# Kernel optimization log

Measured on AMD Instinct MI355X. Metric: run time of the kernel, lower is better.

## Reference

```python
import jax, jax.numpy as jnp
import numpy as np

S = 64        # num_states
ODIM = 8      # padded neighbor-feature width
H = 256       # HIDDEN_DIM
A = 16        # num_actions
B = 16384     # batch (dtpt)
IDIM = S + ODIM
NEG_SLOPE = 0.01  # nn.LeakyReLU default
EPS = 1e-5        # nn.LayerNorm default


def setup_inputs() -> dict:
    key = jax.random.key(0)
    ks = jax.random.split(key, 8)
    x = jax.random.normal(ks[0], (B, S), jnp.float32)
    # per-state neighbor indices into x's feature dim, padded to ODIM with a mask
    o_idx = jax.random.randint(ks[1], (S, ODIM), 0, S)
    o_len = jax.random.randint(ks[2], (S,), 1, ODIM + 1)
    o_mask = jnp.arange(ODIM)[None, :] < o_len[:, None]  # [S, ODIM] bool

    def lin(k, fin, fout):
        bound = 1.0 / np.sqrt(fin)
        kw, kb = jax.random.split(k)
        W = jax.random.uniform(kw, (S, fin, fout), jnp.float32, -bound, bound)
        b = jax.random.uniform(kb, (S, fout), jnp.float32, -bound, bound)
        return W, b

    W1, b1 = lin(ks[3], IDIM, H)
    W2, b2 = lin(ks[4], H, H)
    Wp, bp = lin(ks[5], H, A)
    g1 = jnp.ones((S, H), jnp.float32); be1 = jnp.zeros((S, H), jnp.float32)
    g2 = jnp.ones((S, H), jnp.float32); be2 = jnp.zeros((S, H), jnp.float32)
    return dict(x=x, o_idx=o_idx, o_mask=o_mask, W1=W1, b1=b1, g1=g1, be1=be1,
                W2=W2, b2=b2, g2=g2, be2=be2, Wp=Wp, bp=bp)


def _layer_norm(h, g, b):
    # h: [B, S, H], per-state affine params g,b: [S, H]
    mu = jnp.mean(h, axis=-1, keepdims=True)
    var = jnp.mean((h - mu) ** 2, axis=-1, keepdims=True)
    return (h - mu) * jax.lax.rsqrt(var + EPS) * g[None] + b[None]


def reference(x, o_idx, o_mask, W1, b1, g1, be1, W2, b2, g2, be2, Wp, bp):
    # irregular gather: for each state s take x[:, o_nbr_index[s]], zero-pad to ODIM
    o = jnp.where(o_mask[None, :, :], x[:, o_idx], jnp.float32(0))  # [B, S, ODIM]
    one_hot = jnp.broadcast_to(jnp.eye(S, dtype=x.dtype)[None], (x.shape[0], S, S))
    inp = jnp.concatenate([one_hot, o], axis=-1)  # [B, S, IDIM]

    h = jnp.einsum('bsi,sih->bsh', inp, W1) + b1[None]
    h = _layer_norm(jax.nn.leaky_relu(h, NEG_SLOPE), g1, be1)
    h = jnp.einsum('bsh,shk->bsk', h, W2) + b2[None]
    h = _layer_norm(jax.nn.leaky_relu(h, NEG_SLOPE), g2, be2)
    pi_logit = jnp.einsum('bsh,sha->bsa', h, Wp) + bp[None]  # [B, S, A]
    lg_sm = jax.nn.log_softmax(pi_logit, axis=-1)
    return pi_logit, lg_sm
```

## Files before the change

### kernel.cpp

```cpp
#include <hip/hip_runtime.h>

#define LNEPS 1e-5f

typedef __attribute__((ext_vector_type(8)))  short          bf16x8;
typedef __attribute__((ext_vector_type(8)))  unsigned short u16x8;
typedef __attribute__((ext_vector_type(4)))  float          f32x4;
typedef __attribute__((ext_vector_type(16))) float          f32x16;
typedef __attribute__((ext_vector_type(4)))  unsigned int   u32x4;

#define MFMA32(a, b, c) __builtin_amdgcn_mfma_f32_32x32x16_bf16((a), (b), (c), 0, 0, 0)

#define WS_W2G  0
#define WS_A1   8388608
#define WS_WPG  8912896
#define WS_UC2  10027008
#define WS_MIDX 10092544
#define WS_XG   10094592

union U8 { bf16x8 v; unsigned u[4]; };

__device__ __forceinline__ unsigned short f2bf(float v) {
  union { float f; unsigned u; } a; a.f = v;
  unsigned r = a.u + 0x7fffu + ((a.u >> 16) & 1u);
  return (unsigned short)(r >> 16);
}
__device__ __forceinline__ unsigned cvtpk(float lo, float hi) {
  unsigned r;
  asm("v_cvt_pk_bf16_f32 %0, %1, %2" : "=v"(r) : "v"(lo), "v"(hi));
  return r;
}
__device__ __forceinline__ void swap2(unsigned& a, unsigned& b) {
  asm volatile("v_permlane32_swap_b32 %0, %1" : "+v"(a), "+v"(b));
}

__global__ void prep_midx_k(const int* __restrict__ oidx,
                            const unsigned* __restrict__ mask32,
                            int* __restrict__ midx) {
  __shared__ int fgt1, ffl;
  const int t = threadIdx.x;
  if (t == 0) { fgt1 = 0; ffl = 0; }
  __syncthreads();
  if (t < 128) {
    unsigned wv = mask32[t];
    if (wv == 0x3f800000u) atomicOr(&ffl, 1);
    else if (wv > 1u)      atomicOr(&fgt1, 1);
  }
  __syncthreads();
  const int mode = ffl ? 2 : (fgt1 ? 1 : 0);
  int mv;
  if (mode == 2)      mv = (((const float*)mask32)[t] != 0.0f) ? 1 : 0;
  else if (mode == 1) mv = (int)((const unsigned char*)mask32)[t];
  else                mv = ((const int*)mask32)[t];
  midx[t] = (mv != 0) ? oidx[t] : -1;
}

__global__ __launch_bounds__(256) void prep_xg_k(
    const float* __restrict__ x, const int* __restrict__ midx,
    u32x4* __restrict__ xg) {
  const int g = blockIdx.x * 256 + threadIdx.x;
  const int s = g >> 14, row = g & 16383;
  const float* xr = x + (size_t)row * 64;
  const int* mi = midx + s * 8;
  u32x4 w;
#pragma unroll
  for (int p = 0; p < 4; ++p) {
    const int m0 = mi[2 * p], m1 = mi[2 * p + 1];
    const float a = m0 < 0 ? 0.f : xr[m0];
    const float b = m1 < 0 ? 0.f : xr[m1];
    w[p] = (unsigned)f2bf(a) | ((unsigned)f2bf(b) << 16);
  }
  xg[g] = w;
}

__global__ __launch_bounds__(256) void prep_w2g_k(
    const float* __restrict__ W2, const float* __restrict__ g1,
    unsigned short* __restrict__ w2g) {
  const int tid = blockIdx.x * 256 + threadIdx.x;
  const int l = tid & 63;
  const int t = (tid >> 6) & 15;
  const int i = (tid >> 10) & 7;
  const int s = tid >> 13;
  const int n = i * 32 + (l & 31);
  const int h = l >> 5;
  const float* w = W2 + (size_t)s * 65536;
  const float* g = g1 + s * 256;
  u16x8 v;
#pragma unroll
  for (int j = 0; j < 8; ++j) {
    const int k = t * 16 + h * 8 + j;
    v[j] = f2bf(w[k * 256 + n] * g[k]);
  }
  ((u16x8*)w2g)[tid] = v;
}

__global__ __launch_bounds__(256) void prep_uc2_k(
    const float* __restrict__ W2, const float* __restrict__ g1,
    const float* __restrict__ be1, const float* __restrict__ b2,
    unsigned* __restrict__ uc2) {
  const int tid = blockIdx.x * 256 + threadIdx.x;
  const int s = tid >> 8, n = tid & 255;
  const float* w = W2 + (size_t)s * 65536 + n;
  const float* g = g1 + s * 256;
  const float* be = be1 + s * 256;
  float u = 0.f, c = 0.f;
#pragma unroll 8
  for (int k = 0; k < 256; ++k) {
    const float wk = w[k * 256];
    u = fmaf(wk, g[k], u);
    c = fmaf(wk, be[k], c);
  }
  c += b2[tid];
  uc2[tid] = (unsigned)f2bf(u) | ((unsigned)f2bf(c) << 16);
}

__global__ __launch_bounds__(256) void prep_a1_k(
    const float* __restrict__ W1, const float* __restrict__ b1,
    unsigned short* __restrict__ a1b) {
  const int tid = blockIdx.x * 256 + threadIdx.x;
  const int l = tid & 63;
  const int i = (tid >> 6) & 7;
  const int s = tid >> 9;
  const int n = i * 32 + (l & 31);
  const float* w = W1 + (size_t)s * 72 * 256;
  u16x8 v;
#pragma unroll
  for (int j = 0; j < 8; ++j) v[j] = 0;
  if (l < 32) {
#pragma unroll
    for (int j = 0; j < 8; ++j) v[j] = f2bf(w[(64 + j) * 256 + n]);
  } else {
    v[0] = f2bf(w[s * 256 + n] + b1[s * 256 + n]);
  }
  ((u16x8*)a1b)[tid] = v;
}

__global__ __launch_bounds__(256) void prep_wpg_k(
    const float* __restrict__ Wp, const float* __restrict__ g2,
    const float* __restrict__ be2, const float* __restrict__ bp,
    unsigned short* __restrict__ wpg) {
  const int tid = blockIdx.x * 256 + threadIdx.x;
  const int l = tid & 63;
  const int r = tid >> 6;
  const int t = r % 17;
  const int s = r / 17;
  const int a = l & 31;
  const int h = l >> 5;
  u16x8 v;
#pragma unroll
  for (int j = 0; j < 8; ++j) v[j] = 0;
  if (t < 16) {
    if (a < 16) {
      const float* w = Wp + (size_t)s * 4096;
      const float* g = g2 + s * 256;
#pragma unroll
      for (int j = 0; j < 8; ++j) {
        const int k = t * 16 + h * 8 + j;
        v[j] = f2bf(w[k * 16 + a] * g[k]);
      }
    }
  } else if (h == 0 && a < 16) {
    const float* w = Wp + (size_t)s * 4096;
    float up = 0.f, cp = 0.f;
#pragma unroll 8
    for (int k = 0; k < 256; ++k) {
      const float wk = w[k * 16 + a];
      up = fmaf(wk, g2[s * 256 + k], up);
      cp = fmaf(wk, be2[s * 256 + k], cp);
    }
    cp += bp[s * 16 + a];
    v[0] = f2bf(up); v[1] = f2bf(cp);
  }
  ((u16x8*)wpg)[tid] = v;
}

__device__ __forceinline__ void pack_tile(const f32x16& a,
                                          unsigned* f0, unsigned* f1) {
  unsigned w0 = cvtpk(a[0], a[1]),   w1 = cvtpk(a[2], a[3]);
  unsigned w2 = cvtpk(a[4], a[5]),   w3 = cvtpk(a[6], a[7]);
  unsigned w4 = cvtpk(a[8], a[9]),   w5 = cvtpk(a[10], a[11]);
  unsigned w6 = cvtpk(a[12], a[13]), w7 = cvtpk(a[14], a[15]);
  swap2(w0, w2); swap2(w1, w3); swap2(w4, w6); swap2(w5, w7);
  f0[0] = w0; f0[1] = w1; f0[2] = w2; f0[3] = w3;
  f1[0] = w4; f1[1] = w5; f1[2] = w6; f1[3] = w7;
}

__global__ __launch_bounds__(512, 2) void actor_main(
    const u32x4* __restrict__ xg,
    const unsigned short* __restrict__ w2g, const unsigned* __restrict__ uc2,
    const unsigned short* __restrict__ a1b, const unsigned short* __restrict__ wpg,
    float* __restrict__ out) {
  extern __shared__ char lds[];
  const int tid = threadIdx.x;
  const int wv = tid >> 6;
  const int l = tid & 63;
  const int bl = l & 31;
  const int h = l >> 5;
  const int s = blockIdx.x >> 2;
  const int rowstart = (blockIdx.x & 3) << 12;

  {
    const u32x4* src = (const u32x4*)(w2g + (size_t)s * 65536);
    u32x4* dst = (u32x4*)lds;
#pragma unroll
    for (int i = 0; i < 16; ++i) dst[i * 512 + tid] = src[i * 512 + tid];
  }

  unsigned aext[8];
#pragma unroll
  for (int i = 0; i < 8; ++i) {
    const unsigned t = uc2[(s * 8 + i) * 32 + bl];
    aext[i] = h ? 0u : t;
  }
  const bf16x8* A1 = ((const bf16x8*)a1b) + (size_t)(s * 8) * 64 + l;
  const bf16x8* A3 = ((const bf16x8*)wpg) + (size_t)(s * 17) * 64 + l;
  const char* ldsl = lds + (l << 4);
  const u32x4* XG = xg + ((size_t)s << 14);

  const int rbase = rowstart + wv * 32 + bl;

  u32x4 gcur = XG[rbase];

  __syncthreads();

  for (int it = 0; it < 16; ++it) {
    const int row = rbase + it * 256;

    U8 B1;
    B1.u[0] = h ? 0x00003F80u : gcur[0];
    B1.u[1] = h ? 0u : gcur[1];
    B1.u[2] = h ? 0u : gcur[2];
    B1.u[3] = h ? 0u : gcur[3];

    gcur = XG[rbase + ((it + 1) & 15) * 256];

    float s0 = 0.f, s1 = 0.f, q0 = 0.f, q1 = 0.f;
    f32x16 acc2[8];
    bf16x8 a1n = A1[64];
    bf16x8 Afc[8];
#pragma unroll
    for (int j = 0; j < 8; ++j)
      Afc[j] = *(const bf16x8*)(ldsl + ((j * 16 + 0) << 10));

    f32x16 accP;
    { f32x16 z = {}; accP = MFMA32(A1[0], B1.v, z); }

#pragma unroll
    for (int i = 0; i < 8; ++i) {
      f32x16 yv;
#pragma unroll
      for (int r = 0; r < 16; ++r) {
        float v = accP[r];
        v = fmaxf(v, 0.01f * v);
        yv[r] = v;
        if (r & 1) { s1 += v; q1 = fmaf(v, v, q1); }
        else       { s0 += v; q0 = fmaf(v, v, q0); }
      }
      U8 Bf0, Bf1;
      pack_tile(yv, Bf0.u, Bf1.u);

      if (i < 7) {
        f32x16 z = {};
        accP = MFMA32(a1n, B1.v, z);
        if (i < 6) a1n = A1[(i + 2) * 64];
      }

#pragma unroll
      for (int j = 0; j < 8; ++j) {
        if (i == 0) { f32x16 zz = {}; acc2[j] = MFMA32(Afc[j], Bf0.v, zz); }
        else        { acc2[j] = MFMA32(Afc[j], Bf0.v, acc2[j]); }
      }
      bf16x8 Afn[8];
#pragma unroll
      for (int j = 0; j < 8; ++j)
        Afn[j] = *(const bf16x8*)(ldsl + ((j * 16 + 2 * i + 1) << 10));
#pragma unroll
      for (int j = 0; j < 8; ++j) acc2[j] = MFMA32(Afn[j], Bf1.v, acc2[j]);
      if (i < 7) {
#pragma unroll
        for (int j = 0; j < 8; ++j)
          Afc[j] = *(const bf16x8*)(ldsl + ((j * 16 + 2 * i + 2) << 10));
      }
    }

    float sum = s0 + s1, ssq = q0 + q1;
    sum += __shfl_xor(sum, 32, 64);
    ssq += __shfl_xor(ssq, 32, 64);
    const float m1 = sum * 0.00390625f;
    const float var1 = fmaf(ssq, 0.00390625f, -m1 * m1) + LNEPS;
    const float rho1 = rsqrtf(var1);
    const float std1 = var1 * rho1;
    const unsigned be2w = cvtpk(-m1, std1);
    bf16x8 p0 = A3[0], p1 = A3[64];
    {
      U8 Bx; Bx.u[0] = h ? 0u : be2w; Bx.u[1] = 0; Bx.u[2] = 0; Bx.u[3] = 0;
#pragma unroll
      for (int i = 0; i < 8; ++i) {
        U8 Ax; Ax.u[0] = aext[i]; Ax.u[1] = 0; Ax.u[2] = 0; Ax.u[3] = 0;
        acc2[i] = MFMA32(Ax.v, Bx.v, acc2[i]);
      }
    }

    f32x16 a3a = {}, a3b = {};
    s0 = s1 = q0 = q1 = 0.f;
#pragma unroll
    for (int i = 0; i < 8; ++i) {
      bf16x8 n0, n1;
      if (i < 7) { n0 = A3[(2 * i + 2) * 64]; n1 = A3[(2 * i + 3) * 64]; }
      else       { n0 = A3[16 * 64]; n1 = p1; }
      f32x16 yv;
#pragma unroll
      for (int r = 0; r < 16; ++r) {
        float v = acc2[i][r];
        v = fmaxf(v, 0.01f * v);
        yv[r] = v;
        if (r & 1) { s1 += v; q1 = fmaf(v, v, q1); }
        else       { s0 += v; q0 = fmaf(v, v, q0); }
      }
      U8 Bf0, Bf1;
      pack_tile(yv, Bf0.u, Bf1.u);
      a3a = MFMA32(p0, Bf0.v, a3a);
      a3b = MFMA32(p1, Bf1.v, a3b);
      p0 = n0; p1 = n1;
    }
    float sum2 = s0 + s1, ssq2 = q0 + q1;
    sum2 += __shfl_xor(sum2, 32, 64);
    ssq2 += __shfl_xor(ssq2, 32, 64);
    const float mp = sum2 * 0.00390625f;
    const float qp = ssq2 * 0.00390625f;
    const float var2 = rho1 * rho1 * fmaf(-mp, mp, qp) + LNEPS;
    const float rho2 = rsqrtf(var2);
    const float sigma = rho1 * rho2;
    const float inv = var2 * rho2 * std1;
    const unsigned be3w = cvtpk(-mp, inv);
    {
      U8 Bx; Bx.u[0] = h ? 0u : be3w; Bx.u[1] = 0; Bx.u[2] = 0; Bx.u[3] = 0;
      a3a = MFMA32(p0, Bx.v, a3a);
    }

    float lg[8];
#pragma unroll
    for (int r = 0; r < 8; ++r) lg[r] = sigma * (a3a[r] + a3b[r]);
    float mx = fmaxf(fmaxf(fmaxf(lg[0], lg[1]), fmaxf(lg[2], lg[3])),
                     fmaxf(fmaxf(lg[4], lg[5]), fmaxf(lg[6], lg[7])));
    mx = fmaxf(mx, __shfl_xor(mx, 32, 64));
    float es = 0.f;
#pragma unroll
    for (int r = 0; r < 8; ++r) es += __expf(lg[r] - mx);
    es += __shfl_xor(es, 32, 64);
    const float lse = mx + __logf(es);

    const size_t ob = (((size_t)row << 6) + s) * 16 + (h << 2);
    f32x4 v0 = {lg[0], lg[1], lg[2], lg[3]};
    f32x4 v1 = {lg[4], lg[5], lg[6], lg[7]};
    *(f32x4*)(out + ob) = v0;
    *(f32x4*)(out + ob + 8) = v1;
    f32x4 w0 = {lg[0] - lse, lg[1] - lse, lg[2] - lse, lg[3] - lse};
    f32x4 w1 = {lg[4] - lse, lg[5] - lse, lg[6] - lse, lg[7] - lse};
    *(f32x4*)(out + 16777216 + ob) = w0;
    *(f32x4*)(out + 16777216 + ob + 8) = w1;
  }
}

extern "C" void kernel_launch(void* const* d_in, const int* in_sizes, int n_in,
                              void* d_out, int out_size, void* d_ws, size_t ws_size,
                              hipStream_t stream) {
  const float* x    = (const float*)d_in[0];
  const int*   oidx = (const int*)d_in[1];
  const unsigned* omask = (const unsigned*)d_in[2];
  const float* W1 = (const float*)d_in[3];
  const float* b1 = (const float*)d_in[4];
  const float* g1 = (const float*)d_in[5];
  const float* be1 = (const float*)d_in[6];
  const float* W2 = (const float*)d_in[7];
  const float* b2 = (const float*)d_in[8];
  const float* g2 = (const float*)d_in[9];
  const float* be2 = (const float*)d_in[10];
  const float* Wp = (const float*)d_in[11];
  const float* bp = (const float*)d_in[12];
  float* out = (float*)d_out;

  char* ws = (char*)d_ws;
  unsigned short* wsW2G = (unsigned short*)(ws + WS_W2G);
  unsigned short* wsA1  = (unsigned short*)(ws + WS_A1);
  unsigned short* wsWPG = (unsigned short*)(ws + WS_WPG);
  unsigned*       wsUC2 = (unsigned*)(ws + WS_UC2);
  int*            wsMIDX = (int*)(ws + WS_MIDX);
  u32x4*          wsXG   = (u32x4*)(ws + WS_XG);

  prep_midx_k<<<1, 512, 0, stream>>>(oidx, omask, wsMIDX);
  prep_xg_k<<<4096, 256, 0, stream>>>(x, wsMIDX, wsXG);
  prep_w2g_k<<<2048, 256, 0, stream>>>(W2, g1, wsW2G);
  prep_uc2_k<<<64, 256, 0, stream>>>(W2, g1, be1, b2, wsUC2);
  prep_a1_k<<<128, 256, 0, stream>>>(W1, b1, wsA1);
  prep_wpg_k<<<272, 256, 0, stream>>>(Wp, g2, be2, bp, wsWPG);

  hipFuncSetAttribute((const void*)actor_main,
                      hipFuncAttributeMaxDynamicSharedMemorySize, 131072);
  actor_main<<<256, 512, 131072, stream>>>(
      wsXG, wsW2G, wsUC2, wsA1, wsWPG, out);
}
```

Measured before the change: 288.9 us.

## Use packed f32 math for activation stats, set MFMA priority, nontemporal IO

Replaces the scalar leaky-ReLU plus sum/sum-of-squares loops with packed v_pk_mul/add/fma helpers that handle two elements per instruction. Hoists the second batch of LDS weight-fragment loads ahead of the MFMA block and wraps the MFMAs in s_setprio to favour matrix issue. Switches the gathered-input loads and output stores to nontemporal variants to reduce cache pollution from streaming data. The changes are independent micro-optimisations. Inline asm may restrict compiler scheduling, and hoisting the loads raises register pressure.

```diff
diff --git a/kernel.cpp b/kernel.cpp
--- a/kernel.cpp
+++ b/kernel.cpp
@@ -4,6 +4,7 @@
 
 typedef __attribute__((ext_vector_type(8)))  short          bf16x8;
 typedef __attribute__((ext_vector_type(8)))  unsigned short u16x8;
+typedef __attribute__((ext_vector_type(2)))  float          f32x2;
 typedef __attribute__((ext_vector_type(4)))  float          f32x4;
 typedef __attribute__((ext_vector_type(16))) float          f32x16;
 typedef __attribute__((ext_vector_type(4)))  unsigned int   u32x4;
@@ -31,6 +32,15 @@
 }
 __device__ __forceinline__ void swap2(unsigned& a, unsigned& b) {
   asm volatile("v_permlane32_swap_b32 %0, %1" : "+v"(a), "+v"(b));
+}
+__device__ __forceinline__ f32x2 pk_mul(f32x2 a, f32x2 b) {
+  f32x2 d; asm("v_pk_mul_f32 %0, %1, %2" : "=v"(d) : "v"(a), "v"(b)); return d;
+}
+__device__ __forceinline__ f32x2 pk_add(f32x2 a, f32x2 b) {
+  f32x2 d; asm("v_pk_add_f32 %0, %1, %2" : "=v"(d) : "v"(a), "v"(b)); return d;
+}
+__device__ __forceinline__ f32x2 pk_fma(f32x2 a, f32x2 b, f32x2 c) {
+  f32x2 d; asm("v_pk_fma_f32 %0, %1, %2, %3" : "=v"(d) : "v"(a), "v"(b), "v"(c)); return d;
 }
 
 __global__ void prep_midx_k(const int* __restrict__ oidx,
@@ -184,6 +194,24 @@
   f1[0] = w4; f1[1] = w5; f1[2] = w6; f1[3] = w7;
 }
 
+__device__ __forceinline__ void leaky_stats(const f32x16& acc, f32x16& yv,
+                                            f32x2& s2, f32x2& q2,
+                                            const f32x2 c01) {
+  const f32x2* ap = (const f32x2*)&acc;
+  f32x2* yp = (f32x2*)&yv;
+#pragma unroll
+  for (int m = 0; m < 8; ++m) {
+    const f32x2 v2 = ap[m];
+    const f32x2 m2 = pk_mul(c01, v2);
+    f32x2 y;
+    y.x = fmaxf(v2.x, m2.x);
+    y.y = fmaxf(v2.y, m2.y);
+    yp[m] = y;
+    s2 = pk_add(s2, y);
+    q2 = pk_fma(y, y, q2);
+  }
+}
+
 __global__ __launch_bounds__(512, 2) void actor_main(
     const u32x4* __restrict__ xg,
     const unsigned short* __restrict__ w2g, const unsigned* __restrict__ uc2,
@@ -217,8 +245,9 @@
   const u32x4* XG = xg + ((size_t)s << 14);
 
   const int rbase = rowstart + wv * 32 + bl;
-
-  u32x4 gcur = XG[rbase];
+  const f32x2 c01 = {0.01f, 0.01f};
+
+  u32x4 gcur = __builtin_nontemporal_load(&XG[rbase]);
 
   __syncthreads();
 
@@ -231,9 +260,9 @@
     B1.u[2] = h ? 0u : gcur[2];
     B1.u[3] = h ? 0u : gcur[3];
 
-    gcur = XG[rbase + ((it + 1) & 15) * 256];
-
-    float s0 = 0.f, s1 = 0.f, q0 = 0.f, q1 = 0.f;
+    gcur = __builtin_nontemporal_load(&XG[rbase + ((it + 1) & 15) * 256]);
+
+    f32x2 s2 = {0.f, 0.f}, q2 = {0.f, 0.f};
     f32x16 acc2[8];
     bf16x8 a1n = A1[64];
     bf16x8 Afc[8];
@@ -247,14 +276,7 @@
 #pragma unroll
     for (int i = 0; i < 8; ++i) {
       f32x16 yv;
-#pragma unroll
-      for (int r = 0; r < 16; ++r) {
-        float v = accP[r];
-        v = fmaxf(v, 0.01f * v);
-        yv[r] = v;
-        if (r & 1) { s1 += v; q1 = fmaf(v, v, q1); }
-        else       { s0 += v; q0 = fmaf(v, v, q0); }
-      }
+      leaky_stats(accP, yv, s2, q2, c01);
       U8 Bf0, Bf1;
       pack_tile(yv, Bf0.u, Bf1.u);
 
@@ -264,17 +286,21 @@
         if (i < 6) a1n = A1[(i + 2) * 64];
       }
 
+      bf16x8 Afn[8];
+#pragma unroll
+      for (int j = 0; j < 8; ++j)
+        Afn[j] = *(const bf16x8*)(ldsl + ((j * 16 + 2 * i + 1) << 10));
+
+      __builtin_amdgcn_s_setprio(1);
 #pragma unroll
       for (int j = 0; j < 8; ++j) {
         if (i == 0) { f32x16 zz = {}; acc2[j] = MFMA32(Afc[j], Bf0.v, zz); }
         else        { acc2[j] = MFMA32(Afc[j], Bf0.v, acc2[j]); }
       }
-      bf16x8 Afn[8];
-#pragma unroll
-      for (int j = 0; j < 8; ++j)
-        Afn[j] = *(const bf16x8*)(ldsl + ((j * 16 + 2 * i + 1) << 10));
 #pragma unroll
       for (int j = 0; j < 8; ++j) acc2[j] = MFMA32(Afn[j], Bf1.v, acc2[j]);
+      __builtin_amdgcn_s_setprio(0);
+
       if (i < 7) {
 #pragma unroll
         for (int j = 0; j < 8; ++j)
@@ -282,7 +308,7 @@
       }
     }
 
-    float sum = s0 + s1, ssq = q0 + q1;
+    float sum = s2.x + s2.y, ssq = q2.x + q2.y;
     sum += __shfl_xor(sum, 32, 64);
     ssq += __shfl_xor(ssq, 32, 64);
     const float m1 = sum * 0.00390625f;
@@ -301,28 +327,21 @@
     }
 
     f32x16 a3a = {}, a3b = {};
-    s0 = s1 = q0 = q1 = 0.f;
+    s2.x = 0.f; s2.y = 0.f; q2.x = 0.f; q2.y = 0.f;
 #pragma unroll
     for (int i = 0; i < 8; ++i) {
       bf16x8 n0, n1;
       if (i < 7) { n0 = A3[(2 * i + 2) * 64]; n1 = A3[(2 * i + 3) * 64]; }
       else       { n0 = A3[16 * 64]; n1 = p1; }
       f32x16 yv;
-#pragma unroll
-      for (int r = 0; r < 16; ++r) {
-        float v = acc2[i][r];
-        v = fmaxf(v, 0.01f * v);
-        yv[r] = v;
-        if (r & 1) { s1 += v; q1 = fmaf(v, v, q1); }
-        else       { s0 += v; q0 = fmaf(v, v, q0); }
-      }
+      leaky_stats(acc2[i], yv, s2, q2, c01);
       U8 Bf0, Bf1;
       pack_tile(yv, Bf0.u, Bf1.u);
       a3a = MFMA32(p0, Bf0.v, a3a);
       a3b = MFMA32(p1, Bf1.v, a3b);
       p0 = n0; p1 = n1;
     }
-    float sum2 = s0 + s1, ssq2 = q0 + q1;
+    float sum2 = s2.x + s2.y, ssq2 = q2.x + q2.y;
     sum2 += __shfl_xor(sum2, 32, 64);
     ssq2 += __shfl_xor(ssq2, 32, 64);
     const float mp = sum2 * 0.00390625f;
@@ -352,12 +371,12 @@
     const size_t ob = (((size_t)row << 6) + s) * 16 + (h << 2);
     f32x4 v0 = {lg[0], lg[1], lg[2], lg[3]};
     f32x4 v1 = {lg[4], lg[5], lg[6], lg[7]};
-    *(f32x4*)(out + ob) = v0;
-    *(f32x4*)(out + ob + 8) = v1;
+    __builtin_nontemporal_store(v0, (f32x4*)(out + ob));
+    __builtin_nontemporal_store(v1, (f32x4*)(out + ob + 8));
     f32x4 w0 = {lg[0] - lse, lg[1] - lse, lg[2] - lse, lg[3] - lse};
     f32x4 w1 = {lg[4] - lse, lg[5] - lse, lg[6] - lse, lg[7] - lse};
-    *(f32x4*)(out + 16777216 + ob) = w0;
-    *(f32x4*)(out + 16777216 + ob + 8) = w1;
+    __builtin_nontemporal_store(w0, (f32x4*)(out + 16777216 + ob));
+    __builtin_nontemporal_store(w1, (f32x4*)(out + 16777216 + ob + 8));
   }
 }
 
```

Measured after the change: 313.0 us. 1.08x slower.
